# Kernel tuning notes

Hardware: AMD Instinct MI355X
Metric: run time of the kernel (lower is better)

The kernel has to match this reference:

```python
import jax, jax.numpy as jnp
import numpy as np

B, S, D = 128, 50, 128
NUM_NODE = 40000
HOP, N_ITER, SAMPLE = 2, 2, 12
N_NEI = 8
TEMP, MU, LEAK = 0.5, 0.1, 0.2


def setup_inputs() -> dict:
    key = jax.random.key(0)
    ks = jax.random.split(key, 32)
    stdv = 1.0 / np.sqrt(D)
    u = lambda k, shp: jax.random.uniform(k, shp, jnp.float32, -stdv, stdv)
    return {
        "inputs": jax.random.randint(ks[0], (B, S), 0, NUM_NODE),
        "adj": jax.random.randint(ks[1], (B, S, S), 0, 5),
        "item": jax.random.randint(ks[2], (B, S), 0, NUM_NODE),
        "simi_mask": jax.random.randint(ks[3], (B, S, S), 0, 2),
        "as_items_0": jax.random.randint(ks[4], (B, S, N_NEI), 0, NUM_NODE),
        "as_items_1": jax.random.randint(ks[5], (B, S, N_NEI), 0, NUM_NODE),
        "as_items_ssl_0": jax.random.randint(ks[6], (B, S, N_NEI), 0, NUM_NODE),
        "as_items_ssl_1": jax.random.randint(ks[7], (B, S, N_NEI), 0, NUM_NODE),
        "last_item_mask": jnp.zeros((B, S), bool).at[:, -1].set(True),
        "adj_all": jax.random.randint(ks[8], (NUM_NODE, SAMPLE), 0, NUM_NODE),
        "num": jax.random.uniform(ks[9], (NUM_NODE, SAMPLE)),
        "emb": u(ks[10], (NUM_NODE, D)),
        "pos_emb": u(ks[11], (200, D)),
        "a_local": u(ks[12], (N_ITER, 4, D)),
        "mir_w1": u(ks[13], (N_ITER, D, D)),
        "mir_w2": u(ks[14], (N_ITER, D, D)),
        "glob_w1": u(ks[15], (HOP, D + 1, D)),
        "glob_w2": u(ks[16], (HOP, D, 1)),
        "glob_w3": u(ks[17], (HOP, 2 * D, D)),
        "attr_w": u(ks[18], (2 * D, D)),
        "highway_w": u(ks[19], (2 * D, D)),
        "glu1_w": u(ks[20], (D, D)),
        "glu2_w": u(ks[21], (D, D)),
        "glu4_w": u(ks[22], (D, D)),
        "glu4_b": u(ks[23], (D,)),
        "w_s": u(ks[24], (D, 1)),
        "gate_w": u(ks[25], (2 * D, D)),
    }


def _forward(num, emb, pos_emb, a_local, mir_w1, mir_w2, glob_w1, glob_w2, glob_w3,
             attr_w, highway_w, glu1_w, glu2_w, glu4_w, glu4_b, w_s, gate_w,
             inputs, adj, item, simi_mask, as_lists, as_ssl_lists, last_item_mask, adj_all):
    mi = (inputs != 0).astype(emb.dtype)  # [B,S]
    h = emb[inputs]                        # [B,S,D]

    # ---- AttributeAggregator (masked-mean pool per attribute + gated fusion) ----
    def pool(idx_list):
        ps = []
        for idx in idx_list:
            m = (idx != 0).astype(emb.dtype)[..., None]  # [B,S,N,1]
            ps.append(jnp.sum(emb[idx] * m, 2) / (jnp.sum(m, 2) + 1e-8))
        return jnp.mean(jnp.stack(ps), 0)  # [B,S,D]
    hf1 = pool(as_lists)
    hf2 = pool(as_ssl_lists)
    g_attr = jax.nn.sigmoid(jnp.concatenate([h, hf1], -1) @ attr_w)
    hf = g_attr * h + (1.0 - g_attr) * hf1

    # ---- multi-hop neighbor sampling (irregular gathers) ----
    neigh = [inputs]
    wts = []
    for _ in range(HOP):
        flat = neigh[-1].reshape(-1)
        neigh.append(adj_all[flat].reshape(B, -1))
        wts.append(num[flat].reshape(B, -1))
    ev = [emb[n] for n in neigh]  # [B,S,D], [B,S*12,D], [B,S*144,D]

    item_emb = emb[item] * mi[..., None]
    sess = jnp.sum(item_emb, 1) / jnp.sum(mi, -1, keepdims=True)  # [B,D]

    # ---- GlobalAggregator stack (GCE-GNN style attention over sampled neighbors) ----
    for n_hop in range(HOP):
        nxt = []
        for hop in range(HOP - n_hop):
            sv = ev[hop]                                   # [B,M,D]
            nv = ev[hop + 1].reshape(B, -1, SAMPLE, D)     # [B,M,12,D]
            nw = wts[hop].reshape(B, -1, SAMPLE)           # [B,M,12]
            extra = jnp.broadcast_to(sess[:, None, None, :], nv.shape)
            a = jnp.concatenate([extra * nv, nw[..., None]], -1)  # [B,M,12,D+1]
            a = jax.nn.leaky_relu(a @ glob_w1[n_hop], LEAK)
            a = jax.nn.softmax((a @ glob_w2[n_hop])[..., 0], -1)[..., None]
            agg = jnp.sum(a * nv, -2)
            nxt.append(jnp.tanh(jnp.concatenate([sv, agg], -1) @ glob_w3[n_hop]))
        ev = nxt
    h_global = ev[0].reshape(B, S, D)

    # ---- LocalAggregator (edge-typed GAT) + MirrorAggregator (gated exchange) ----
    x = h
    mirror = hf
    for i in range(HOP):
        e = jax.nn.leaky_relu(jnp.einsum('bid,bjd,kd->kbij', x, x, a_local[i]), LEAK)
        att = jnp.full((B, S, S), -9e15, x.dtype)
        for k in range(4):
            att = jnp.where(adj == k + 1, e[k], att)
        x = jax.nn.softmax(att, -1) @ x
        gm = jax.nn.sigmoid(x @ mir_w1[i] + mirror @ mir_w2[i])
        x, mirror = gm * x + (1.0 - gm) * mirror, gm * mirror + (1.0 - gm) * x

    # ---- highway + last-item select ----
    g = jax.nn.sigmoid(jnp.concatenate([h, x], -1) @ highway_w)
    x_dot = g * h + (1.0 - g) * x
    h_local = jnp.sum(x_dot * last_item_mask[..., None].astype(x_dot.dtype), 1)  # [B,D]

    mask = mi[..., None]
    pos = pos_emb[:S][None]  # [1,S,D]
    bw = emb[1:]             # [NUM_NODE-1,D]
    hs = jnp.sum(h_global * mask, -2) / jnp.sum(mask, 1)  # [B,D]

    # ---- SSL pairwise similarity loss ----
    sim = jnp.einsum('bid,bjd->bij', hf1, hf2) / TEMP
    l = -jnp.log(jax.nn.softmax(sim, 2) + 1e-8)
    simi_loss = jnp.mean(jnp.sum(l * (simi_mask == 1), (1, 2)))

    # ---- attention-style GLU scoring ----
    hp = x_dot + pos
    nh = jax.nn.sigmoid(hp @ glu1_w + hs[:, None, :] @ glu2_w + h_local[:, None, :] @ glu4_w + glu4_b)
    beta = (nh @ w_s) * mask
    zg = jnp.sum(beta * hp, 1)  # [B,D]
    gf = jax.nn.sigmoid(jnp.concatenate([zg, h_local], -1) @ gate_w) * MU
    zh = gf * h_local + (1.0 - gf) * zg
    scores = zh @ bw.T  # [B, NUM_NODE-1]
    return simi_loss, scores


def reference(inputs, adj, item, simi_mask, as_items_0, as_items_1,
              as_items_ssl_0, as_items_ssl_1, last_item_mask, adj_all, num,
              emb, pos_emb, a_local, mir_w1, mir_w2, glob_w1, glob_w2, glob_w3,
              attr_w, highway_w, glu1_w, glu2_w, glu4_w, glu4_b, w_s, gate_w):
    return _forward(num, emb, pos_emb, a_local, mir_w1, mir_w2, glob_w1, glob_w2, glob_w3,
                    attr_w, highway_w, glu1_w, glu2_w, glu4_w, glu4_b, w_s, gate_w,
                    inputs, adj, item, simi_mask, [as_items_0, as_items_1],
                    [as_items_ssl_0, as_items_ssl_1], last_item_mask, adj_all)
```

## Files before the change

### kernel.cpp

```cpp
#include <hip/hip_runtime.h>
#include <hip/hip_bf16.h>
#include <type_traits>


#define B 128
#define S 50
#define D 128
#define SAMPLE 12
#define NNEI 8
#define NODES 40000
#define NSC (NODES - 1)
#define LEAK 0.2f
#define TEMPV 0.5f
#define MUV 0.1f
#define NEG_BIG -3.0e38f

typedef const float* fpp;
typedef float* fpw;
typedef unsigned short u16;
typedef __attribute__((ext_vector_type(8))) short bfrag8;
typedef __attribute__((ext_vector_type(4))) float f32x4;

__device__ __forceinline__ float sigm(float x) { return 1.f / (1.f + __expf(-x)); }
__device__ __forceinline__ float tanh_f(float x) { return 1.f - 2.f / (__expf(2.f * x) + 1.f); }
__device__ __forceinline__ float leaky(float x) { return x >= 0.f ? x : LEAK * x; }
__device__ __forceinline__ u16 f2bf(float v) {
  __hip_bfloat16 h = __float2bfloat16(v);
  return *reinterpret_cast<u16*>(&h);
}
__device__ __forceinline__ float lde(const float* p, long i) { return p[i]; }
__device__ __forceinline__ float lde(const u16* p, long i) {
  union { unsigned int u; float f; } c;
  c.u = ((unsigned int)p[i]) << 16;
  return c.f;
}

__global__ __launch_bounds__(256) void kprep_emb(fpp emb, u16* __restrict__ out) {
  long i = ((long)blockIdx.x * 256 + threadIdx.x) * 4;
  if (i + 3 >= (long)NODES * D) return;
  float4 v = *(const float4*)(emb + i);
  out[i + 0] = f2bf(v.x); out[i + 1] = f2bf(v.y);
  out[i + 2] = f2bf(v.z); out[i + 3] = f2bf(v.w);
}

__global__ __launch_bounds__(256) void kprep4(fpp gw1, fpp gw3,
                                              u16* __restrict__ p1a,
                                              u16* __restrict__ p1b,
                                              u16* __restrict__ p3a,
                                              u16* __restrict__ p3b) {
  int i = blockIdx.x * 256 + threadIdx.x;
  fpp W; u16* dst; int KS;
  if (i < 16384)      { W = gw1;             dst = p1a; KS = 4; }
  else if (i < 32768) { W = gw1 + 129 * 128; dst = p1b; KS = 4; i -= 16384; }
  else if (i < 65536) { W = gw3;             dst = p3a; KS = 8; i -= 32768; }
  else                { W = gw3 + 256 * 128; dst = p3b; KS = 8; i -= 65536; }
  int e = i & 7;
  int lane = (i >> 3) & 63;
  int rest = i >> 9;
  int ks = rest % KS, nt = rest / KS;
  int k = ks * 32 + ((lane >> 4) << 3) + e;
  int n = (nt << 4) + (lane & 15);
  dst[i] = f2bf(W[(long)k * 128 + n]);
}

template <typename ET>
__global__ __launch_bounds__(128) void k1_gather(
    const int* __restrict__ inputs, const int* __restrict__ as0,
// ... 20 lines not shown
  }
  float hf1v = 0.5f * (p[0] + p[1]);
  float hf2v = 0.5f * (p[2] + p[3]);
  h_s[d] = hv;
  hf1_s[d] = hf1v;
  __syncthreads();
  float acc = 0.f;
  for (int k = 0; k < D; k++)
    acc += h_s[k] * attr_w[(long)k * D + d] + hf1_s[k] * attr_w[(long)(D + k) * D + d];
  float g = sigm(acc);
  float hfv = g * hv + (1.f - g) * hf1v;
  long o = (long)bs * D + d;
  h[o] = hv; hf1[o] = hf1v; hf2[o] = hf2v; xA[o] = hv; mir[o] = hfv;
  if (d == 0) mi[bs] = (inp != 0) ? 1.f : 0.f;
}

__global__ __launch_bounds__(128) void k2_sess(const int* __restrict__ inputs,
                                               const int* __restrict__ item,
                                               fpp emb, fpw sess) {
  int b = blockIdx.x;
  int d = threadIdx.x;
  float acc = 0.f, ms = 0.f;
  for (int s = 0; s < S; s++) {
    int inp = inputs[b * S + s];
    float m = (inp != 0) ? 1.f : 0.f;
    int it = item[b * S + s];
    acc += emb[(long)it * D + d] * m;
    ms += m;
  }
  sess[(long)b * D + d] = acc / ms;
}

template <typename ET>
__global__ __launch_bounds__(128) void kG_global(
    const int* __restrict__ inputs, const int* __restrict__ adj_all,
    fpp num, const ET* __restrict__ emb, fpp sess,
    fpp W1a, fpp W2a, fpp W1b, fpp W2b, fpp W3b,
    const u16* __restrict__ p1a, const u16* __restrict__ p1b,
    const u16* __restrict__ p3a, const u16* __restrict__ p3b,
    fpw hg) {
  int bs = blockIdx.x;
  int b = bs / S;
  int d = threadIdx.x;
  int lane = d & 63;
  int w = d >> 6;
  int q = lane >> 4;
  int mrow = lane & 15;

  __shared__ __align__(16) u16 nvs_l[16 * 136];
  __shared__ __align__(16) u16 svagg_l[16 * 264];
  __shared__ __align__(16) float ev_l[13 * 128];
  __shared__ __align__(16) float agg1_l[128];
  __shared__ float red_l[2][16];
  __shared__ float nw_l[16];

#pragma unroll
  for (int r = 12; r < 16; r++) {
    nvs_l[r * 136 + d] = 0;
    if (d < 8) nvs_l[r * 136 + 128 + d] = 0;
  }
#pragma unroll
  for (int r = 13; r < 16; r++) {
    svagg_l[r * 264 + d] = 0;
    svagg_l[r * 264 + 128 + d] = 0;
    if (d < 8) svagg_l[r * 264 + 256 + d] = 0;
  }

  float sess_d = sess[(long)b * D + d];
  int src0 = __builtin_amdgcn_readfirstlane(inputs[bs]);
  int n1[SAMPLE];
#pragma unroll
  for (int j = 0; j < SAMPLE; j++)
    n1[j] = __builtin_amdgcn_readfirstlane(adj_all[(long)src0 * SAMPLE + j]);
  svagg_l[0 * 264 + d] = f2bf(lde(emb, (long)src0 * D + d));

  float w2A[4], wlA[4], w2B[4], wlB[4];
#pragma unroll
  for (int nt = 0; nt < 4; nt++) {
    int col = (w * 4 + nt) * 16 + mrow;
    w2A[nt] = W2a[col];
    wlA[nt] = W1a[(long)D * D + col];
    w2B[nt] = W2b[col];
    wlB[nt] = W1b[(long)D * D + col];
  }

  float pre[SAMPLE], pnw = 0.f;
  {
#pragma unroll
    for (int j = 0; j < SAMPLE; j++)
      pre[j] = lde(emb, (long)n1[j] * D + d);
    if (d < SAMPLE) pnw = num[(long)src0 * SAMPLE + d];
  }
  for (int u = 0; u < 13; u++) {
    if (d < SAMPLE) nw_l[d] = pnw;
    float nvreg[SAMPLE];
#pragma unroll
    for (int j = 0; j < SAMPLE; j++) {
      nvreg[j] = pre[j];
      nvs_l[j * 136 + d] = f2bf(pre[j] * sess_d);
    }
    if (u == 0) {
#pragma unroll
      for (int j = 0; j < SAMPLE; j++)
        svagg_l[(1 + j) * 264 + d] = f2bf(nvreg[j]);
    }
    __syncthreads();
    if (u < 12) {
      int srcn = n1[u];
#pragma unroll
      for (int j = 0; j < SAMPLE; j++) {
        int nj = __builtin_amdgcn_readfirstlane(adj_all[(long)srcn * SAMPLE + j]);
        pre[j] = lde(emb, (long)nj * D + d);
      }
      if (d < SAMPLE) pnw = num[(long)srcn * SAMPLE + d];
    }
    f32x4 acc[4];
#pragma unroll
    for (int nt = 0; nt < 4; nt++) acc[nt] = (f32x4){0.f, 0.f, 0.f, 0.f};
#pragma unroll
    for (int ks = 0; ks < 4; ks++) {
      bfrag8 a = *(const bfrag8*)(nvs_l + mrow * 136 + q * 8 + ks * 32);
      const u16* pb = p1a + (w * 16 + ks) * 512 + lane * 8;
#pragma unroll
      for (int nt = 0; nt < 4; nt++) {
        bfrag8 bb = *(const bfrag8*)(pb + nt * 2048);
        acc[nt] = __builtin_amdgcn_mfma_f32_16x16x32_bf16(a, bb, acc[nt], 0, 0, 0);
      }
    }
    float lp[4] = {0.f, 0.f, 0.f, 0.f};
    float nwq[4];
#pragma unroll
    for (int i = 0; i < 4; i++) nwq[i] = (q < 3) ? nw_l[q * 4 + i] : 0.f;
#pragma unroll
    for (int nt = 0; nt < 4; nt++)
#pragma unroll
      for (int i = 0; i < 4; i++)
        lp[i] += leaky(acc[nt][i] + nwq[i] * wlA[nt]) * w2A[nt];
#pragma unroll
    for (int off = 1; off <= 8; off <<= 1)
#pragma unroll
      for (int i = 0; i < 4; i++) lp[i] += __shfl_xor(lp[i], off, 64);
    if (mrow == 0 && q < 3) {
#pragma unroll
      for (int i = 0; i < 4; i++) red_l[w][q * 4 + i] = lp[i];
    }
    __syncthreads();
    float lg[SAMPLE];
#pragma unroll
    for (int j = 0; j < SAMPLE; j++) lg[j] = red_l[0][j] + red_l[1][j];
    float mx = lg[0];
#pragma unroll
    for (int j = 1; j < SAMPLE; j++) mx = fmaxf(mx, lg[j]);
    float se = 0.f;
#pragma unroll
    for (int j = 0; j < SAMPLE; j++) { lg[j] = __expf(lg[j] - mx); se += lg[j]; }
    float inv = 1.f / se;
    float aggd = 0.f;
#pragma unroll
    for (int j = 0; j < SAMPLE; j++) aggd += lg[j] * inv * nvreg[j];
    svagg_l[u * 264 + 128 + d] = f2bf(aggd);
  }
  __syncthreads();

  {
    f32x4 accB[4];
#pragma unroll
    for (int nt = 0; nt < 4; nt++) accB[nt] = (f32x4){0.f, 0.f, 0.f, 0.f};
#pragma unroll
    for (int ks = 0; ks < 8; ks++) {
      bfrag8 a = *(const bfrag8*)(svagg_l + mrow * 264 + q * 8 + ks * 32);
      const u16* pb = p3a + (w * 32 + ks) * 512 + lane * 8;
#pragma unroll
      for (int nt = 0; nt < 4; nt++) {
        bfrag8 bb = *(const bfrag8*)(pb + nt * 4096);
        accB[nt] = __builtin_amdgcn_mfma_f32_16x16x32_bf16(a, bb, accB[nt], 0, 0, 0);
      }
    }
#pragma unroll
    for (int nt = 0; nt < 4; nt++) {
      int col = (w * 4 + nt) * 16 + mrow;
#pragma unroll
      for (int i = 0; i < 4; i++) {
        int u2 = q * 4 + i;
        if (u2 < 13) ev_l[u2 * 128 + col] = tanh_f(accB[nt][i]);
      }
    }
    __syncthreads();
  }

  {
    float evreg[SAMPLE];
#pragma unroll
    for (int j = 0; j < SAMPLE; j++) {
      float e = ev_l[(1 + j) * 128 + d];
      evreg[j] = e;
      nvs_l[j * 136 + d] = f2bf(e * sess_d);
    }
    if (d < SAMPLE) nw_l[d] = num[(long)src0 * SAMPLE + d];
    __syncthreads();

    f32x4 acc[4];
#pragma unroll
    for (int nt = 0; nt < 4; nt++) acc[nt] = (f32x4){0.f, 0.f, 0.f, 0.f};
#pragma unroll
    for (int ks = 0; ks < 4; ks++) {
      bfrag8 a = *(const bfrag8*)(nvs_l + mrow * 136 + q * 8 + ks * 32);
      const u16* pb = p1b + (w * 16 + ks) * 512 + lane * 8;
#pragma unroll
      for (int nt = 0; nt < 4; nt++) {
        bfrag8 bb = *(const bfrag8*)(pb + nt * 2048);
        acc[nt] = __builtin_amdgcn_mfma_f32_16x16x32_bf16(a, bb, acc[nt], 0, 0, 0);
      }
    }
    float lp[4] = {0.f, 0.f, 0.f, 0.f};
    float nwq[4];
#pragma unroll
    for (int i = 0; i < 4; i++) nwq[i] = (q < 3) ? nw_l[q * 4 + i] : 0.f;
#pragma unroll
    for (int nt = 0; nt < 4; nt++)
#pragma unroll
      for (int i = 0; i < 4; i++)
        lp[i] += leaky(acc[nt][i] + nwq[i] * wlB[nt]) * w2B[nt];
#pragma unroll
    for (int off = 1; off <= 8; off <<= 1)
#pragma unroll
      for (int i = 0; i < 4; i++) lp[i] += __shfl_xor(lp[i], off, 64);
    if (mrow == 0 && q < 3) {
#pragma unroll
      for (int i = 0; i < 4; i++) red_l[w][q * 4 + i] = lp[i];
    }
    __syncthreads();

    float lg[SAMPLE];
#pragma unroll
    for (int j = 0; j < SAMPLE; j++) lg[j] = red_l[0][j] + red_l[1][j];
    float mx = lg[0];
#pragma unroll
    for (int j = 1; j < SAMPLE; j++) mx = fmaxf(mx, lg[j]);
    float se = 0.f;
#pragma unroll
    for (int j = 0; j < SAMPLE; j++) { lg[j] = __expf(lg[j] - mx); se += lg[j]; }
    float inv = 1.f / se;
    float agg1d = 0.f;
#pragma unroll
    for (int j = 0; j < SAMPLE; j++) agg1d += lg[j] * inv * evreg[j];
    agg1_l[d] = agg1d;
    __syncthreads();

    float accf = 0.f;
#pragma unroll 4
    for (int k4 = 0; k4 < 32; k4++) {
      float4 a4 = *(const float4*)&ev_l[4 * k4];
      float4 g4 = *(const float4*)&agg1_l[4 * k4];
      accf += a4.x * W3b[(4 * k4 + 0) * D + d] + a4.y * W3b[(4 * k4 + 1) * D + d] +
              a4.z * W3b[(4 * k4 + 2) * D + d] + a4.w * W3b[(4 * k4 + 3) * D + d] +
              g4.x * W3b[(D + 4 * k4 + 0) * D + d] + g4.y * W3b[(D + 4 * k4 + 1) * D + d] +
              g4.z * W3b[(D + 4 * k4 + 2) * D + d] + g4.w * W3b[(D + 4 * k4 + 3) * D + d];
    }
    hg[(long)bs * D + d] = tanh_f(accf);
  }
}

__global__ __launch_bounds__(128) void k5ab(fpp x, const int* __restrict__ adj,
                                            fpp a_loc, fpp w1, fpp w2,
                                            fpw xout, fpw mir,
                                            fpp hw, fpp h, fpw x_dot,
                                            float* __restrict__ h_local,
                                            int fin) {
  int b = blockIdx.x / S;
  int row = blockIdx.x % S;
  int tid = threadIdx.x;
  __shared__ float xi_s[D];
  __shared__ float ak_s[4][D];
  __shared__ float alpha_s[S];
  __shared__ float part_s[4][2][64];
  long idx = ((long)b * S + row) * D + tid;
  xi_s[tid] = x[idx];
#pragma unroll
  for (int k = 0; k < 4; k++) ak_s[k][tid] = a_loc[(long)k * D + tid];
  __syncthreads();
  {
    int j = tid & 63, hf = tid >> 6;
    float a0 = 0.f, a1 = 0.f, a2 = 0.f, a3 = 0.f;
    if (j < S) {
      const float* xj = x + ((long)b * S + j) * D + hf * 64;
      int off = hf * 64;
      for (int dd = 0; dd < 64; dd++) {
        float prod = xi_s[off + dd] * xj[dd];
        a0 += prod * ak_s[0][off + dd];
        a1 += prod * ak_s[1][off + dd];
        a2 += prod * ak_s[2][off + dd];
        a3 += prod * ak_s[3][off + dd];
      }
// ... 243 lines not shown
  fpp mir_w2 = (fpp)d_in[15];
  fpp gw1 = (fpp)d_in[16];
  fpp gw2 = (fpp)d_in[17];
  fpp gw3 = (fpp)d_in[18];
  fpp attr_w = (fpp)d_in[19];
  fpp highway_w = (fpp)d_in[20];
  fpp glu1 = (fpp)d_in[21];
  fpp glu2 = (fpp)d_in[22];
  fpp glu4 = (fpp)d_in[23];
  fpp glu4b = (fpp)d_in[24];
  fpp w_s = (fpp)d_in[25];
  fpp gate_w = (fpp)d_in[26];

  float* ob = (float*)d_out;
  constexpr long BSD_ = (long)B * S * D;
  fpw s_h = ob + 0 * BSD_;
  fpw s_hf1 = ob + 1 * BSD_;
  fpw s_hf2 = ob + 2 * BSD_;
  fpw s_mir = ob + 3 * BSD_;
  fpw s_xA = ob + 4 * BSD_;
  fpw s_xB = ob + 5 * BSD_;

  float* ws = (float*)d_ws;
  float* w_loss = ws + 0;
  float* w_mi = ws + 16;
  float* w_sess = w_mi + (long)B * S;
  float* w_hl = w_sess + (long)B * D;
  float* w_zh = w_hl + (long)B * D;
  u16* p1a = (u16*)(ws + 72000);
  u16* p1b = (u16*)(ws + 72000 + 8192);
  u16* p3a = (u16*)(ws + 72000 + 16384);
  u16* p3b = (u16*)(ws + 72000 + 32768);
  u16* embbf = (u16*)((char*)d_ws + 491520);
  bool useBF = ws_size >= (size_t)12 * 1024 * 1024;

  hipMemsetAsync((void*)w_loss, 0, sizeof(float), stream);

  kprep4<<<384, 256, 0, stream>>>(gw1, gw3, p1a, p1b, p3a, p3b);
  if (useBF)
    kprep_emb<<<(NODES * D / 4 + 255) / 256, 256, 0, stream>>>(emb, embbf);

  if (useBF)
    k1_gather<u16><<<B * S, 128, 0, stream>>>(inputs, as0, as1, ss0, ss1,
                                              embbf, attr_w, s_h, s_hf1, s_hf2,
                                              w_mi, s_xA, s_mir);
  else
    k1_gather<float><<<B * S, 128, 0, stream>>>(inputs, as0, as1, ss0, ss1,
                                                emb, attr_w, s_h, s_hf1, s_hf2,
                                                w_mi, s_xA, s_mir);
  k7_simi<<<B * S, 128, 0, stream>>>(s_hf1, s_hf2, simi_mask, w_loss);
  k2_sess<<<B, 128, 0, stream>>>(inputs, item, emb, w_sess);
  if (useBF)
    kG_global<u16><<<B * S, 128, 0, stream>>>(inputs, adj_all, num, embbf,
                                              w_sess, gw1, gw2,
                                              gw1 + 129 * 128, gw2 + 128,
                                              gw3 + 256 * 128, p1a, p1b, p3a,
                                              p3b, s_hf2 );
  else
    kG_global<float><<<B * S, 128, 0, stream>>>(inputs, adj_all, num, emb,
                                                w_sess, gw1, gw2,
                                                gw1 + 129 * 128, gw2 + 128,
                                                gw3 + 256 * 128, p1a, p1b, p3a,
                                                p3b, s_hf2 );
  k5ab<<<B * S, 128, 0, stream>>>(s_xA, adj, a_local, mir_w1, mir_w2,
                                  s_xB, s_mir, highway_w, s_h, s_hf1, w_hl, 0);
  k5ab<<<B * S, 128, 0, stream>>>(s_xB, adj, a_local + 4 * D,
                                  mir_w1 + (long)D * D, mir_w2 + (long)D * D,
                                  s_xA, s_mir, highway_w, s_h,
                                  s_hf1 , w_hl, 1);
  k8_glu<<<B, 512, 0, stream>>>(s_hf2 , s_hf1 , pos,
                                w_hl, w_mi, glu1, glu2, glu4, glu4b, w_s,
                                gate_w, w_zh);
  if (useBF)
    k9_scores<u16><<<(NSC + 63) / 64, 256, 0, stream>>>(w_zh, embbf, w_loss,
                                                        (float*)d_out);
  else
    k9_scores<float><<<(NSC + 63) / 64, 256, 0, stream>>>(w_zh, emb, w_loss,
                                                          (float*)d_out);
}
```

Baseline: 739.6 us.

## Restructure global aggregator kernel: 4 waves each own neighbor groups, prefetch indices

The global-graph kernel now runs 256 threads (4 waves). All second-hop neighbor indices and weights are prefetched into shared memory up front. Each wave independently processes a subset of the 13 neighbor groups with its own MFMA tile covering the full 128 output columns and a wave-local softmax, which removes the per-iteration block barriers. Gathered rows are loaded directly as bf16 MFMA fragments with double buffering, and the final linear layer is split across both thread halves. The cost is more registers per thread (launch bounds set to 3 blocks) and redundant weight-fragment loads per wave.

```diff
diff --git a/kernel.cpp b/kernel.cpp
--- a/kernel.cpp
+++ b/kernel.cpp
@@ -33,6 +33,37 @@
   union { unsigned int u; float f; } c;
   c.u = ((unsigned int)p[i]) << 16;
   return c.f;
+}
+__device__ __forceinline__ float bfu(short s) {
+  union { unsigned u; float f; } c;
+  c.u = ((unsigned)(unsigned short)s) << 16;
+  return c.f;
+}
+
+template <typename ET>
+__device__ __forceinline__ bfrag8 load_frag(const ET* __restrict__ emb, long row, int koff) {
+  if constexpr (sizeof(ET) == 2) {
+    return *(const bfrag8*)(const void*)(emb + row * D + koff);
+  } else {
+    const float* s = (const float*)(emb + row * D + koff);
+    float4 lo = *(const float4*)s;
+    float4 hi = *(const float4*)(s + 4);
+    bfrag8 b;
+    b[0] = (short)f2bf(lo.x); b[1] = (short)f2bf(lo.y);
+    b[2] = (short)f2bf(lo.z); b[3] = (short)f2bf(lo.w);
+    b[4] = (short)f2bf(hi.x); b[5] = (short)f2bf(hi.y);
+    b[6] = (short)f2bf(hi.z); b[7] = (short)f2bf(hi.w);
+    return b;
+  }
+}
+
+__device__ __forceinline__ bfrag8 scale8(bfrag8 r, float4 sa, float4 sb) {
+  bfrag8 o;
+  o[0] = (short)f2bf(bfu(r[0]) * sa.x); o[1] = (short)f2bf(bfu(r[1]) * sa.y);
+  o[2] = (short)f2bf(bfu(r[2]) * sa.z); o[3] = (short)f2bf(bfu(r[3]) * sa.w);
+  o[4] = (short)f2bf(bfu(r[4]) * sb.x); o[5] = (short)f2bf(bfu(r[5]) * sb.y);
+  o[6] = (short)f2bf(bfu(r[6]) * sb.z); o[7] = (short)f2bf(bfu(r[7]) * sb.w);
+  return o;
 }
 
 __global__ __launch_bounds__(256) void kprep_emb(fpp emb, u16* __restrict__ out) {
@@ -119,233 +150,246 @@
 }
 
 template <typename ET>
-__global__ __launch_bounds__(128) void kG_global(
+__global__ __launch_bounds__(256, 3) void kG_global(
     const int* __restrict__ inputs, const int* __restrict__ adj_all,
     fpp num, const ET* __restrict__ emb, fpp sess,
     fpp W1a, fpp W2a, fpp W1b, fpp W2b, fpp W3b,
     const u16* __restrict__ p1a, const u16* __restrict__ p1b,
-    const u16* __restrict__ p3a, const u16* __restrict__ p3b,
-    fpw hg) {
+    const u16* __restrict__ p3a, fpw hg) {
   int bs = blockIdx.x;
   int b = bs / S;
-  int d = threadIdx.x;
-  int lane = d & 63;
-  int w = d >> 6;
+  int t = threadIdx.x;
+  int lane = t & 63;
+  int w = t >> 6;
   int q = lane >> 4;
   int mrow = lane & 15;
 
-  __shared__ __align__(16) u16 nvs_l[16 * 136];
-  __shared__ __align__(16) u16 svagg_l[16 * 264];
-  __shared__ __align__(16) float ev_l[13 * 128];
+  __shared__ int n1_l[12];
+  __shared__ int idx_l[160];
+  __shared__ __align__(16) float nw_l[160];
+  __shared__ int svidx_l[16];
+  __shared__ __align__(16) u16 nvs_l[4][16 * 136];
+  __shared__ __align__(16) u16 agg_l[16 * 136];
+  __shared__ __align__(16) float ev_l[16 * 132];
+  __shared__ float red_l[64];
   __shared__ __align__(16) float agg1_l[128];
-  __shared__ float red_l[2][16];
-  __shared__ float nw_l[16];
-
-#pragma unroll
-  for (int r = 12; r < 16; r++) {
-    nvs_l[r * 136 + d] = 0;
-    if (d < 8) nvs_l[r * 136 + 128 + d] = 0;
-  }
-#pragma unroll
-  for (int r = 13; r < 16; r++) {
-    svagg_l[r * 264 + d] = 0;
-    svagg_l[r * 264 + 128 + d] = 0;
-    if (d < 8) svagg_l[r * 264 + 256 + d] = 0;
-  }
-
-  float sess_d = sess[(long)b * D + d];
-  int src0 = __builtin_amdgcn_readfirstlane(inputs[bs]);
-  int n1[SAMPLE];
-#pragma unroll
-  for (int j = 0; j < SAMPLE; j++)
-    n1[j] = __builtin_amdgcn_readfirstlane(adj_all[(long)src0 * SAMPLE + j]);
-  svagg_l[0 * 264 + d] = f2bf(lde(emb, (long)src0 * D + d));
-
-  float w2A[4], wlA[4], w2B[4], wlB[4];
-#pragma unroll
-  for (int nt = 0; nt < 4; nt++) {
-    int col = (w * 4 + nt) * 16 + mrow;
-    w2A[nt] = W2a[col];
-    wlA[nt] = W1a[(long)D * D + col];
-    w2B[nt] = W2b[col];
-    wlB[nt] = W1b[(long)D * D + col];
-  }
-
-  float pre[SAMPLE], pnw = 0.f;
+
+  int src0 = inputs[bs];
+  if (t < 12) n1_l[t] = adj_all[(long)src0 * SAMPLE + t];
+  if (t < 204) ((unsigned*)agg_l)[884 + t] = 0;
+  __syncthreads();
+  if (t < 156) {
+    int u = (t * 683) >> 13;
+    int j = t - u * 12;
+    int su = u ? n1_l[u - 1] : src0;
+    idx_l[t] = adj_all[(long)su * SAMPLE + j];
+    nw_l[t] = num[(long)su * SAMPLE + j];
+  } else if (t < 160) {
+    idx_l[t] = 0; nw_l[t] = 0.f;
+  } else if (t < 176) {
+    int m = t - 160;
+    svidx_l[m] = (m == 0) ? src0 : (m <= 12 ? n1_l[m - 1] : 0);
+  }
+  __syncthreads();
+
+  const float* sessb = sess + (long)b * D;
+  float wl8[8], w28[8];
+#pragma unroll
+  for (int nt = 0; nt < 8; nt++) {
+    int col = nt * 16 + mrow;
+    wl8[nt] = W1a[(long)D * D + col];
+    w28[nt] = W2a[col];
+  }
+  u16* nvsw = nvs_l[w];
+
+  bfrag8 rawA[4], rawB[4];
   {
-#pragma unroll
-    for (int j = 0; j < SAMPLE; j++)
-      pre[j] = lde(emb, (long)n1[j] * D + d);
-    if (d < SAMPLE) pnw = num[(long)src0 * SAMPLE + d];
-  }
-  for (int u = 0; u < 13; u++) {
-    if (d < SAMPLE) nw_l[d] = pnw;
-    float nvreg[SAMPLE];
-#pragma unroll
-    for (int j = 0; j < SAMPLE; j++) {
-      nvreg[j] = pre[j];
-      nvs_l[j * 136 + d] = f2bf(pre[j] * sess_d);
-    }
-    if (u == 0) {
-#pragma unroll
-      for (int j = 0; j < SAMPLE; j++)
-        svagg_l[(1 + j) * 264 + d] = f2bf(nvreg[j]);
-    }
-    __syncthreads();
-    if (u < 12) {
-      int srcn = n1[u];
-#pragma unroll
-      for (int j = 0; j < SAMPLE; j++) {
-        int nj = __builtin_amdgcn_readfirstlane(adj_all[(long)srcn * SAMPLE + j]);
-        pre[j] = lde(emb, (long)nj * D + d);
+    long ridx = idx_l[w * 12 + (mrow < 12 ? mrow : 0)];
+#pragma unroll
+    for (int ks = 0; ks < 4; ks++) rawA[ks] = load_frag(emb, ridx, ks * 32 + q * 8);
+  }
+  for (int u = w; u < 13; u += 4) {
+    int un = u + 4;
+    if (un < 13) {
+      long ridx = idx_l[un * 12 + (mrow < 12 ? mrow : 0)];
+#pragma unroll
+      for (int ks = 0; ks < 4; ks++) rawB[ks] = load_frag(emb, ridx, ks * 32 + q * 8);
+    }
+    f32x4 acc[8];
+#pragma unroll
+    for (int nt = 0; nt < 8; nt++) acc[nt] = (f32x4){0.f, 0.f, 0.f, 0.f};
+#pragma unroll
+    for (int ks = 0; ks < 4; ks++) {
+      float4 sa = *(const float4*)(sessb + ks * 32 + q * 8);
+      float4 sb = *(const float4*)(sessb + ks * 32 + q * 8 + 4);
+      bfrag8 a = scale8(rawA[ks], sa, sb);
+      const u16* pb = p1a + ks * 512 + lane * 8;
+#pragma unroll
+      for (int nt = 0; nt < 8; nt++)
+        acc[nt] = __builtin_amdgcn_mfma_f32_16x16x32_bf16(
+            a, *(const bfrag8*)(pb + nt * 2048), acc[nt], 0, 0, 0);
+    }
+    float4 nwq = *(const float4*)(nw_l + u * 12 + q * 4);
+    float lp[4] = {0.f, 0.f, 0.f, 0.f};
+#pragma unroll
+    for (int nt = 0; nt < 8; nt++) {
+      lp[0] += leaky(acc[nt][0] + nwq.x * wl8[nt]) * w28[nt];
+      lp[1] += leaky(acc[nt][1] + nwq.y * wl8[nt]) * w28[nt];
+      lp[2] += leaky(acc[nt][2] + nwq.z * wl8[nt]) * w28[nt];
+      lp[3] += leaky(acc[nt][3] + nwq.w * wl8[nt]) * w28[nt];
+    }
+#pragma unroll
+    for (int off = 1; off <= 8; off <<= 1)
+#pragma unroll
+      for (int i = 0; i < 4; i++) lp[i] += __shfl_xor(lp[i], off, 64);
+    float m4 = (q < 3) ? fmaxf(fmaxf(lp[0], lp[1]), fmaxf(lp[2], lp[3])) : NEG_BIG;
+    m4 = fmaxf(m4, __shfl_xor(m4, 16, 64));
+    m4 = fmaxf(m4, __shfl_xor(m4, 32, 64));
+    float e0 = 0.f, e1 = 0.f, e2 = 0.f, e3 = 0.f, ssum = 0.f;
+    if (q < 3) {
+      e0 = __expf(lp[0] - m4); e1 = __expf(lp[1] - m4);
+      e2 = __expf(lp[2] - m4); e3 = __expf(lp[3] - m4);
+      ssum = e0 + e1 + e2 + e3;
+    }
+    ssum += __shfl_xor(ssum, 16, 64);
+    ssum += __shfl_xor(ssum, 32, 64);
+    float inv = 1.f / ssum;
+    float al[4] = {e0 * inv, e1 * inv, e2 * inv, e3 * inv};
+    float aj[12];
+#pragma unroll
+    for (int j = 0; j < 12; j++) aj[j] = __shfl(al[j & 3], (j >> 2) << 4, 64);
+#pragma unroll
+    for (int ks = 0; ks < 4; ks++)
+      *(bfrag8*)(nvsw + mrow * 136 + ks * 32 + q * 8) = rawA[ks];
+    float a0 = 0.f, a1 = 0.f;
+#pragma unroll
+    for (int j = 0; j < 12; j++) {
+      unsigned pv = *(const unsigned*)(nvsw + j * 136 + lane * 2);
+      union { unsigned u; float f; } lo, hi;
+      lo.u = pv << 16; hi.u = pv & 0xffff0000u;
+      a0 += aj[j] * lo.f; a1 += aj[j] * hi.f;
+    }
+    unsigned pk = ((unsigned)f2bf(a1) << 16) | (unsigned)f2bf(a0);
+    *(unsigned*)(agg_l + u * 136 + lane * 2) = pk;
+#pragma unroll
+    for (int ks = 0; ks < 4; ks++) rawA[ks] = rawB[ks];
+  }
+  __syncthreads();
+
+  {
+    long svr = svidx_l[mrow];
+    f32x4 accB[2];
+    accB[0] = (f32x4){0.f, 0.f, 0.f, 0.f};
+    accB[1] = (f32x4){0.f, 0.f, 0.f, 0.f};
+#pragma unroll
+    for (int ks = 0; ks < 4; ks++) {
+      bfrag8 a = load_frag(emb, svr, ks * 32 + q * 8);
+      const u16* pb = p3a + ks * 512 + lane * 8;
+#pragma unroll
+      for (int n = 0; n < 2; n++)
+        accB[n] = __builtin_amdgcn_mfma_f32_16x16x32_bf16(
+            a, *(const bfrag8*)(pb + (w * 2 + n) * 4096), accB[n], 0, 0, 0);
+    }
+#pragma unroll
+    for (int ks = 4; ks < 8; ks++) {
+      bfrag8 a = *(const bfrag8*)(agg_l + mrow * 136 + (ks - 4) * 32 + q * 8);
+      const u16* pb = p3a + ks * 512 + lane * 8;
+#pragma unroll
+      for (int n = 0; n < 2; n++)
+        accB[n] = __builtin_amdgcn_mfma_f32_16x16x32_bf16(
+            a, *(const bfrag8*)(pb + (w * 2 + n) * 4096), accB[n], 0, 0, 0);
+    }
+#pragma unroll
+    for (int n = 0; n < 2; n++) {
+      int col = (w * 2 + n) * 16 + mrow;
+#pragma unroll
+      for (int i = 0; i < 4; i++) {
+        int row = q * 4 + i;
+        if (row < 13) ev_l[row * 132 + col] = tanh_f(accB[n][i]);
       }
-      if (d < SAMPLE) pnw = num[(long)srcn * SAMPLE + d];
-    }
-    f32x4 acc[4];
-#pragma unroll
-    for (int nt = 0; nt < 4; nt++) acc[nt] = (f32x4){0.f, 0.f, 0.f, 0.f};
+    }
+  }
+  __syncthreads();
+
+  {
+    float wlB[2], w2B[2];
+#pragma unroll
+    for (int n = 0; n < 2; n++) {
+      int col = (w * 2 + n) * 16 + mrow;
+      wlB[n] = W1b[(long)D * D + col];
+      w2B[n] = W2b[col];
+    }
+    int rr = 1 + (mrow < 12 ? mrow : 0);
+    f32x4 accC[2];
+    accC[0] = (f32x4){0.f, 0.f, 0.f, 0.f};
+    accC[1] = (f32x4){0.f, 0.f, 0.f, 0.f};
 #pragma unroll
     for (int ks = 0; ks < 4; ks++) {
-      bfrag8 a = *(const bfrag8*)(nvs_l + mrow * 136 + q * 8 + ks * 32);
-      const u16* pb = p1a + (w * 16 + ks) * 512 + lane * 8;
-#pragma unroll
-      for (int nt = 0; nt < 4; nt++) {
-        bfrag8 bb = *(const bfrag8*)(pb + nt * 2048);
-        acc[nt] = __builtin_amdgcn_mfma_f32_16x16x32_bf16(a, bb, acc[nt], 0, 0, 0);
-      }
-    }
-    float lp[4] = {0.f, 0.f, 0.f, 0.f};
-    float nwq[4];
-#pragma unroll
-    for (int i = 0; i < 4; i++) nwq[i] = (q < 3) ? nw_l[q * 4 + i] : 0.f;
-#pragma unroll
-    for (int nt = 0; nt < 4; nt++)
-#pragma unroll
-      for (int i = 0; i < 4; i++)
-        lp[i] += leaky(acc[nt][i] + nwq[i] * wlA[nt]) * w2A[nt];
+      float4 sa = *(const float4*)(sessb + ks * 32 + q * 8);
+      float4 sb = *(const float4*)(sessb + ks * 32 + q * 8 + 4);
+      float4 lo = *(const float4*)(ev_l + rr * 132 + ks * 32 + q * 8);
+      float4 hi = *(const float4*)(ev_l + rr * 132 + ks * 32 + q * 8 + 4);
+      bfrag8 a;
+      a[0] = (short)f2bf(lo.x * sa.x); a[1] = (short)f2bf(lo.y * sa.y);
+      a[2] = (short)f2bf(lo.z * sa.z); a[3] = (short)f2bf(lo.w * sa.w);
+      a[4] = (short)f2bf(hi.x * sb.x); a[5] = (short)f2bf(hi.y * sb.y);
+      a[6] = (short)f2bf(hi.z * sb.z); a[7] = (short)f2bf(hi.w * sb.w);
+      const u16* pb = p1b + ks * 512 + lane * 8;
+#pragma unroll
+      for (int n = 0; n < 2; n++)
+        accC[n] = __builtin_amdgcn_mfma_f32_16x16x32_bf16(
+            a, *(const bfrag8*)(pb + (w * 2 + n) * 2048), accC[n], 0, 0, 0);
+    }
+    float4 nwq0 = *(const float4*)(nw_l + q * 4);
+    float lp2[4] = {0.f, 0.f, 0.f, 0.f};
+#pragma unroll
+    for (int n = 0; n < 2; n++) {
+      lp2[0] += leaky(accC[n][0] + nwq0.x * wlB[n]) * w2B[n];
+      lp2[1] += leaky(accC[n][1] + nwq0.y * wlB[n]) * w2B[n];
+      lp2[2] += leaky(accC[n][2] + nwq0.z * wlB[n]) * w2B[n];
+      lp2[3] += leaky(accC[n][3] + nwq0.w * wlB[n]) * w2B[n];
+    }
 #pragma unroll
     for (int off = 1; off <= 8; off <<= 1)
 #pragma unroll
-      for (int i = 0; i < 4; i++) lp[i] += __shfl_xor(lp[i], off, 64);
-    if (mrow == 0 && q < 3) {
-#pragma unroll
-      for (int i = 0; i < 4; i++) red_l[w][q * 4 + i] = lp[i];
-    }
-    __syncthreads();
-    float lg[SAMPLE];
-#pragma unroll
-    for (int j = 0; j < SAMPLE; j++) lg[j] = red_l[0][j] + red_l[1][j];
+      for (int i = 0; i < 4; i++) lp2[i] += __shfl_xor(lp2[i], off, 64);
+    if (mrow == 0) {
+#pragma unroll
+      for (int i = 0; i < 4; i++) red_l[w * 16 + q * 4 + i] = lp2[i];
+    }
+  }
+  __syncthreads();
+  {
+    float lg[12];
+#pragma unroll
+    for (int j = 0; j < 12; j++)
+      lg[j] = red_l[j] + red_l[16 + j] + red_l[32 + j] + red_l[48 + j];
     float mx = lg[0];
 #pragma unroll
-    for (int j = 1; j < SAMPLE; j++) mx = fmaxf(mx, lg[j]);
+    for (int j = 1; j < 12; j++) mx = fmaxf(mx, lg[j]);
     float se = 0.f;
 #pragma unroll
-    for (int j = 0; j < SAMPLE; j++) { lg[j] = __expf(lg[j] - mx); se += lg[j]; }
-    float inv = 1.f / se;
-    float aggd = 0.f;
-#pragma unroll
-    for (int j = 0; j < SAMPLE; j++) aggd += lg[j] * inv * nvreg[j];
-    svagg_l[u * 264 + 128 + d] = f2bf(aggd);
-  }
-  __syncthreads();
-
+    for (int j = 0; j < 12; j++) { lg[j] = __expf(lg[j] - mx); se += lg[j]; }
+    float invc = 1.f / se;
+    if (t < 128) {
+      float ag = 0.f;
+#pragma unroll
+      for (int j = 0; j < 12; j++) ag += lg[j] * invc * ev_l[(1 + j) * 132 + t];
+      agg1_l[t] = ag;
+    }
+  }
+  __syncthreads();
   {
-    f32x4 accB[4];
-#pragma unroll
-    for (int nt = 0; nt < 4; nt++) accB[nt] = (f32x4){0.f, 0.f, 0.f, 0.f};
-#pragma unroll
-    for (int ks = 0; ks < 8; ks++) {
-      bfrag8 a = *(const bfrag8*)(svagg_l + mrow * 264 + q * 8 + ks * 32);
-      const u16* pb = p3a + (w * 32 + ks) * 512 + lane * 8;
-#pragma unroll
-      for (int nt = 0; nt < 4; nt++) {
-        bfrag8 bb = *(const bfrag8*)(pb + nt * 4096);
-        accB[nt] = __builtin_amdgcn_mfma_f32_16x16x32_bf16(a, bb, accB[nt], 0, 0, 0);
-      }
-    }
-#pragma unroll
-    for (int nt = 0; nt < 4; nt++) {
-      int col = (w * 4 + nt) * 16 + mrow;
-#pragma unroll
-      for (int i = 0; i < 4; i++) {
-        int u2 = q * 4 + i;
-        if (u2 < 13) ev_l[u2 * 128 + col] = tanh_f(accB[nt][i]);
-      }
-    }
-    __syncthreads();
-  }
-
-  {
-    float evreg[SAMPLE];
-#pragma unroll
-    for (int j = 0; j < SAMPLE; j++) {
-      float e = ev_l[(1 + j) * 128 + d];
-      evreg[j] = e;
-      nvs_l[j * 136 + d] = f2bf(e * sess_d);
-    }
-    if (d < SAMPLE) nw_l[d] = num[(long)src0 * SAMPLE + d];
-    __syncthreads();
-
-    f32x4 acc[4];
-#pragma unroll
-    for (int nt = 0; nt < 4; nt++) acc[nt] = (f32x4){0.f, 0.f, 0.f, 0.f};
-#pragma unroll
-    for (int ks = 0; ks < 4; ks++) {
-      bfrag8 a = *(const bfrag8*)(nvs_l + mrow * 136 + q * 8 + ks * 32);
-      const u16* pb = p1b + (w * 16 + ks) * 512 + lane * 8;
-#pragma unroll
-      for (int nt = 0; nt < 4; nt++) {
-        bfrag8 bb = *(const bfrag8*)(pb + nt * 2048);
-        acc[nt] = __builtin_amdgcn_mfma_f32_16x16x32_bf16(a, bb, acc[nt], 0, 0, 0);
-      }
-    }
-    float lp[4] = {0.f, 0.f, 0.f, 0.f};
-    float nwq[4];
-#pragma unroll
-    for (int i = 0; i < 4; i++) nwq[i] = (q < 3) ? nw_l[q * 4 + i] : 0.f;
-#pragma unroll
-    for (int nt = 0; nt < 4; nt++)
-#pragma unroll
-      for (int i = 0; i < 4; i++)
-        lp[i] += leaky(acc[nt][i] + nwq[i] * wlB[nt]) * w2B[nt];
-#pragma unroll
-    for (int off = 1; off <= 8; off <<= 1)
-#pragma unroll
-      for (int i = 0; i < 4; i++) lp[i] += __shfl_xor(lp[i], off, 64);
-    if (mrow == 0 && q < 3) {
-#pragma unroll
-      for (int i = 0; i < 4; i++) red_l[w][q * 4 + i] = lp[i];
-    }
-    __syncthreads();
-
-    float lg[SAMPLE];
-#pragma unroll
-    for (int j = 0; j < SAMPLE; j++) lg[j] = red_l[0][j] + red_l[1][j];
-    float mx = lg[0];
-#pragma unroll
-    for (int j = 1; j < SAMPLE; j++) mx = fmaxf(mx, lg[j]);
-    float se = 0.f;
-#pragma unroll
-    for (int j = 0; j < SAMPLE; j++) { lg[j] = __expf(lg[j] - mx); se += lg[j]; }
-    float inv = 1.f / se;
-    float agg1d = 0.f;
-#pragma unroll
-    for (int j = 0; j < SAMPLE; j++) agg1d += lg[j] * inv * evreg[j];
-    agg1_l[d] = agg1d;
-    __syncthreads();
-
+    int d = t & 127, hh = t >> 7;
+    const float* av = hh ? agg1_l : ev_l;
+    const float* Wp = W3b + (hh ? (long)128 * D : 0) + d;
     float accf = 0.f;
 #pragma unroll 4
-    for (int k4 = 0; k4 < 32; k4++) {
-      float4 a4 = *(const float4*)&ev_l[4 * k4];
-      float4 g4 = *(const float4*)&agg1_l[4 * k4];
-      accf += a4.x * W3b[(4 * k4 + 0) * D + d] + a4.y * W3b[(4 * k4 + 1) * D + d] +
-              a4.z * W3b[(4 * k4 + 2) * D + d] + a4.w * W3b[(4 * k4 + 3) * D + d] +
-              g4.x * W3b[(D + 4 * k4 + 0) * D + d] + g4.y * W3b[(D + 4 * k4 + 1) * D + d] +
-              g4.z * W3b[(D + 4 * k4 + 2) * D + d] + g4.w * W3b[(D + 4 * k4 + 3) * D + d];
-    }
-    hg[(long)bs * D + d] = tanh_f(accf);
-  }
+    for (int k = 0; k < 128; k++) accf += av[k] * Wp[(long)k * D];
+    ev_l[(14 + hh) * 132 + d] = accf;
+  }
+  __syncthreads();
+  if (t < 128) hg[(long)bs * D + t] = tanh_f(ev_l[14 * 132 + t] + ev_l[15 * 132 + t]);
 }
 
 __global__ __launch_bounds__(128) void k5ab(fpp x, const int* __restrict__ adj,
@@ -674,17 +718,17 @@
   k7_simi<<<B * S, 128, 0, stream>>>(s_hf1, s_hf2, simi_mask, w_loss);
   k2_sess<<<B, 128, 0, stream>>>(inputs, item, emb, w_sess);
   if (useBF)
-    kG_global<u16><<<B * S, 128, 0, stream>>>(inputs, adj_all, num, embbf,
+    kG_global<u16><<<B * S, 256, 0, stream>>>(inputs, adj_all, num, embbf,
                                               w_sess, gw1, gw2,
                                               gw1 + 129 * 128, gw2 + 128,
                                               gw3 + 256 * 128, p1a, p1b, p3a,
-                                              p3b, s_hf2 );
+                                              s_hf2 );
   else
-    kG_global<float><<<B * S, 128, 0, stream>>>(inputs, adj_all, num, emb,
+    kG_global<float><<<B * S, 256, 0, stream>>>(inputs, adj_all, num, emb,
                                                 w_sess, gw1, gw2,
                                                 gw1 + 129 * 128, gw2 + 128,
                                                 gw3 + 256 * 128, p1a, p1b, p3a,
-                                                p3b, s_hf2 );
+                                                s_hf2 );
   k5ab<<<B * S, 128, 0, stream>>>(s_xA, adj, a_local, mir_w1, mir_w2,
                                   s_xB, s_mir, highway_w, s_h, s_hf1, w_hl, 0);
   k5ab<<<B * S, 128, 0, stream>>>(s_xB, adj, a_local + 4 * D,
```

After: 1.160 ms. 56.9% more time.

## Split global aggregator into per-unit hop-1 kernel and post-processing kernel

Applied to the files above, without the earlier changes.

Replaces the monolithic global-aggregation kernel with two kernels. The first launches one 64-thread block per (session position, neighbor unit), 13 per position, to compute the first-hop neighbor attention and aggregation with MFMA, writing bf16 results to a workspace. The second consumes those results to do the second hop, softmax and output projection with 256-thread blocks. The aim is more parallelism and occupancy in exchange for an extra launch and a workspace round trip. The split path only runs when the workspace is at least 32 MB.

```diff
diff --git a/kernel.cpp b/kernel.cpp
--- a/kernel.cpp
+++ b/kernel.cpp
@@ -33,6 +33,37 @@
   union { unsigned int u; float f; } c;
   c.u = ((unsigned int)p[i]) << 16;
   return c.f;
+}
+__device__ __forceinline__ float bfu(short s) {
+  union { unsigned u; float f; } c;
+  c.u = ((unsigned)(unsigned short)s) << 16;
+  return c.f;
+}
+
+template <typename ET>
+__device__ __forceinline__ bfrag8 load_frag(const ET* __restrict__ emb, long row, int koff) {
+  if constexpr (sizeof(ET) == 2) {
+    return *(const bfrag8*)(const void*)(emb + row * D + koff);
+  } else {
+    const float* s = (const float*)(emb + row * D + koff);
+    float4 lo = *(const float4*)s;
+    float4 hi = *(const float4*)(s + 4);
+    bfrag8 b;
+    b[0] = (short)f2bf(lo.x); b[1] = (short)f2bf(lo.y);
+    b[2] = (short)f2bf(lo.z); b[3] = (short)f2bf(lo.w);
+    b[4] = (short)f2bf(hi.x); b[5] = (short)f2bf(hi.y);
+    b[6] = (short)f2bf(hi.z); b[7] = (short)f2bf(hi.w);
+    return b;
+  }
+}
+
+__device__ __forceinline__ bfrag8 scale8(bfrag8 r, float4 sa, float4 sb) {
+  bfrag8 o;
+  o[0] = (short)f2bf(bfu(r[0]) * sa.x); o[1] = (short)f2bf(bfu(r[1]) * sa.y);
+  o[2] = (short)f2bf(bfu(r[2]) * sa.z); o[3] = (short)f2bf(bfu(r[3]) * sa.w);
+  o[4] = (short)f2bf(bfu(r[4]) * sb.x); o[5] = (short)f2bf(bfu(r[5]) * sb.y);
+  o[6] = (short)f2bf(bfu(r[6]) * sb.z); o[7] = (short)f2bf(bfu(r[7]) * sb.w);
+  return o;
 }
 
 __global__ __launch_bounds__(256) void kprep_emb(fpp emb, u16* __restrict__ out) {
@@ -119,13 +150,256 @@
 }
 
 template <typename ET>
-__global__ __launch_bounds__(128) void kG_global(
+__global__ __launch_bounds__(64) void kGA_unit(
+    const int* __restrict__ inputs, const int* __restrict__ adj_all,
+    fpp num, const ET* __restrict__ emb, fpp sess,
+    fpp W1a, fpp W2a, const u16* __restrict__ p1a,
+    u16* __restrict__ aggws) {
+  int gb = blockIdx.x;
+  int bs = gb / 13;
+  int u = gb - bs * 13;
+  int b = bs / S;
+  int lane = threadIdx.x;
+  int q = lane >> 4;
+  int mrow = lane & 15;
+
+  __shared__ __align__(16) u16 nvs[16 * 136];
+
+  int src0 = inputs[bs];
+  int srcu = (u == 0) ? src0 : adj_all[(long)src0 * SAMPLE + (u - 1)];
+  int rid = adj_all[(long)srcu * SAMPLE + (mrow < 12 ? mrow : 0)];
+  float nwq[4];
+#pragma unroll
+  for (int i = 0; i < 4; i++)
+    nwq[i] = (q < 3) ? num[(long)srcu * SAMPLE + q * 4 + i] : 0.f;
+
+  const float* sessb = sess + (long)b * D;
+  bfrag8 rawA[4], sA[4];
+#pragma unroll
+  for (int ks = 0; ks < 4; ks++)
+    rawA[ks] = load_frag(emb, (long)rid, ks * 32 + q * 8);
+#pragma unroll
+  for (int ks = 0; ks < 4; ks++)
+    *(bfrag8*)(nvs + mrow * 136 + ks * 32 + q * 8) = rawA[ks];
+#pragma unroll
+  for (int ks = 0; ks < 4; ks++) {
+    float4 sa = *(const float4*)(sessb + ks * 32 + q * 8);
+    float4 sb = *(const float4*)(sessb + ks * 32 + q * 8 + 4);
+    sA[ks] = scale8(rawA[ks], sa, sb);
+  }
+  float wl8[8], w28[8];
+#pragma unroll
+  for (int nt = 0; nt < 8; nt++) {
+    int col = nt * 16 + mrow;
+    wl8[nt] = W1a[(long)D * D + col];
+    w28[nt] = W2a[col];
+  }
+  float lp[4] = {0.f, 0.f, 0.f, 0.f};
+#pragma unroll
+  for (int nt = 0; nt < 8; nt++) {
+    f32x4 acc = (f32x4){0.f, 0.f, 0.f, 0.f};
+#pragma unroll
+    for (int ks = 0; ks < 4; ks++)
+      acc = __builtin_amdgcn_mfma_f32_16x16x32_bf16(
+          sA[ks], *(const bfrag8*)(p1a + ks * 512 + lane * 8 + nt * 2048), acc, 0, 0, 0);
+    lp[0] += leaky(acc[0] + nwq[0] * wl8[nt]) * w28[nt];
+    lp[1] += leaky(acc[1] + nwq[1] * wl8[nt]) * w28[nt];
+    lp[2] += leaky(acc[2] + nwq[2] * wl8[nt]) * w28[nt];
+    lp[3] += leaky(acc[3] + nwq[3] * wl8[nt]) * w28[nt];
+  }
+#pragma unroll
+  for (int off = 1; off <= 8; off <<= 1)
+#pragma unroll
+    for (int i = 0; i < 4; i++) lp[i] += __shfl_xor(lp[i], off, 64);
+  float m4 = (q < 3) ? fmaxf(fmaxf(lp[0], lp[1]), fmaxf(lp[2], lp[3])) : NEG_BIG;
+  m4 = fmaxf(m4, __shfl_xor(m4, 16, 64));
+  m4 = fmaxf(m4, __shfl_xor(m4, 32, 64));
+  float e0 = 0.f, e1 = 0.f, e2 = 0.f, e3 = 0.f, ssum = 0.f;
+  if (q < 3) {
+    e0 = __expf(lp[0] - m4); e1 = __expf(lp[1] - m4);
+    e2 = __expf(lp[2] - m4); e3 = __expf(lp[3] - m4);
+    ssum = e0 + e1 + e2 + e3;
+  }
+  ssum += __shfl_xor(ssum, 16, 64);
+  ssum += __shfl_xor(ssum, 32, 64);
+  float inv = 1.f / ssum;
+  float al[4] = {e0 * inv, e1 * inv, e2 * inv, e3 * inv};
+  float aj[12];
+#pragma unroll
+  for (int j = 0; j < 12; j++) aj[j] = __shfl(al[j & 3], (j >> 2) << 4, 64);
+  float a0 = 0.f, a1 = 0.f;
+#pragma unroll
+  for (int j = 0; j < 12; j++) {
+    unsigned pv = *(const unsigned*)(nvs + j * 136 + lane * 2);
+    union { unsigned u; float f; } lo, hi;
+    lo.u = pv << 16; hi.u = pv & 0xffff0000u;
+    a0 += aj[j] * lo.f; a1 += aj[j] * hi.f;
+  }
+  unsigned pk = ((unsigned)f2bf(a1) << 16) | (unsigned)f2bf(a0);
+  *(unsigned*)(aggws + ((long)bs * 13 + u) * 128 + lane * 2) = pk;
+}
+
+template <typename ET>
+__global__ __launch_bounds__(256) void kGB_post(
+    const int* __restrict__ inputs, const int* __restrict__ adj_all,
+    fpp num, const ET* __restrict__ emb, fpp sess,
+    fpp W1b, fpp W2b, fpp W3b,
+    const u16* __restrict__ p1b, const u16* __restrict__ p3a,
+    const u16* __restrict__ aggws, fpw hg) {
+  int bs = blockIdx.x;
+  int b = bs / S;
+  int t = threadIdx.x;
+  int lane = t & 63;
+  int w = t >> 6;
+  int q = lane >> 4;
+  int mrow = lane & 15;
+
+  __shared__ int svidx_l[16];
+  __shared__ __align__(16) float ev_l[16 * 132];
+  __shared__ float red_l[64];
+  __shared__ __align__(16) float agg1_l[128];
+
+  int src0 = inputs[bs];
+  if (t < 16)
+    svidx_l[t] = (t == 0) ? src0 : (t <= 12 ? adj_all[(long)src0 * SAMPLE + t - 1] : 0);
+  __syncthreads();
+  const float* sessb = sess + (long)b * D;
+
+  {
+    long svr = svidx_l[mrow];
+    f32x4 accB[2];
+    accB[0] = (f32x4){0.f, 0.f, 0.f, 0.f};
+    accB[1] = (f32x4){0.f, 0.f, 0.f, 0.f};
+#pragma unroll
+    for (int ks = 0; ks < 4; ks++) {
+      bfrag8 a = load_frag(emb, svr, ks * 32 + q * 8);
+      const u16* pb = p3a + ks * 512 + lane * 8;
+#pragma unroll
+      for (int n = 0; n < 2; n++)
+        accB[n] = __builtin_amdgcn_mfma_f32_16x16x32_bf16(
+            a, *(const bfrag8*)(pb + (w * 2 + n) * 4096), accB[n], 0, 0, 0);
+    }
+#pragma unroll
+    for (int ks = 4; ks < 8; ks++) {
+      bfrag8 a;
+      if (mrow < 13)
+        a = *(const bfrag8*)(aggws + ((long)bs * 13 + mrow) * 128 + (ks - 4) * 32 + q * 8);
+      else
+        a = (bfrag8){0, 0, 0, 0, 0, 0, 0, 0};
+      const u16* pb = p3a + ks * 512 + lane * 8;
+#pragma unroll
+      for (int n = 0; n < 2; n++)
+        accB[n] = __builtin_amdgcn_mfma_f32_16x16x32_bf16(
+            a, *(const bfrag8*)(pb + (w * 2 + n) * 4096), accB[n], 0, 0, 0);
+    }
+#pragma unroll
+    for (int n = 0; n < 2; n++) {
+      int col = (w * 2 + n) * 16 + mrow;
+#pragma unroll
+      for (int i = 0; i < 4; i++) {
+        int row = q * 4 + i;
+        if (row < 13) ev_l[row * 132 + col] = tanh_f(accB[n][i]);
+      }
+    }
+  }
+  __syncthreads();
+
+  {
+    float wlB[2], w2B[2];
+#pragma unroll
+    for (int n = 0; n < 2; n++) {
+      int col = (w * 2 + n) * 16 + mrow;
+      wlB[n] = W1b[(long)D * D + col];
+      w2B[n] = W2b[col];
+    }
+    int rr = 1 + (mrow < 12 ? mrow : 0);
+    f32x4 accC[2];
+    accC[0] = (f32x4){0.f, 0.f, 0.f, 0.f};
+    accC[1] = (f32x4){0.f, 0.f, 0.f, 0.f};
+#pragma unroll
+    for (int ks = 0; ks < 4; ks++) {
+      float4 sa = *(const float4*)(sessb + ks * 32 + q * 8);
+      float4 sb = *(const float4*)(sessb + ks * 32 + q * 8 + 4);
+      float4 lo = *(const float4*)(ev_l + rr * 132 + ks * 32 + q * 8);
+      float4 hi = *(const float4*)(ev_l + rr * 132 + ks * 32 + q * 8 + 4);
+      bfrag8 a;
+      a[0] = (short)f2bf(lo.x * sa.x); a[1] = (short)f2bf(lo.y * sa.y);
+      a[2] = (short)f2bf(lo.z * sa.z); a[3] = (short)f2bf(lo.w * sa.w);
+      a[4] = (short)f2bf(hi.x * sb.x); a[5] = (short)f2bf(hi.y * sb.y);
+      a[6] = (short)f2bf(hi.z * sb.z); a[7] = (short)f2bf(hi.w * sb.w);
+      const u16* pb = p1b + ks * 512 + lane * 8;
+#pragma unroll
+      for (int n = 0; n < 2; n++)
+        accC[n] = __builtin_amdgcn_mfma_f32_16x16x32_bf16(
+            a, *(const bfrag8*)(pb + (w * 2 + n) * 2048), accC[n], 0, 0, 0);
+    }
+    float4 nwq0;
+    if (q < 3) {
+      nwq0.x = num[(long)src0 * SAMPLE + q * 4 + 0];
+      nwq0.y = num[(long)src0 * SAMPLE + q * 4 + 1];
+      nwq0.z = num[(long)src0 * SAMPLE + q * 4 + 2];
+      nwq0.w = num[(long)src0 * SAMPLE + q * 4 + 3];
+    } else {
+      nwq0.x = nwq0.y = nwq0.z = nwq0.w = 0.f;
+    }
+    float lp2[4] = {0.f, 0.f, 0.f, 0.f};
+#pragma unroll
+    for (int n = 0; n < 2; n++) {
+      lp2[0] += leaky(accC[n][0] + nwq0.x * wlB[n]) * w2B[n];
+      lp2[1] += leaky(accC[n][1] + nwq0.y * wlB[n]) * w2B[n];
+      lp2[2] += leaky(accC[n][2] + nwq0.z * wlB[n]) * w2B[n];
+      lp2[3] += leaky(accC[n][3] + nwq0.w * wlB[n]) * w2B[n];
+    }
+#pragma unroll
+    for (int off = 1; off <= 8; off <<= 1)
+#pragma unroll
+      for (int i = 0; i < 4; i++) lp2[i] += __shfl_xor(lp2[i], off, 64);
+    if (mrow == 0) {
+#pragma unroll
+      for (int i = 0; i < 4; i++) red_l[w * 16 + q * 4 + i] = lp2[i];
+    }
+  }
+  __syncthreads();
+  {
+    float lg[12];
+#pragma unroll
+    for (int j = 0; j < 12; j++)
+      lg[j] = red_l[j] + red_l[16 + j] + red_l[32 + j] + red_l[48 + j];
+    float mx = lg[0];
+#pragma unroll
+    for (int j = 1; j < 12; j++) mx = fmaxf(mx, lg[j]);
+    float se = 0.f;
+#pragma unroll
+    for (int j = 0; j < 12; j++) { lg[j] = __expf(lg[j] - mx); se += lg[j]; }
+    float invc = 1.f / se;
+    if (t < 128) {
+      float ag = 0.f;
+#pragma unroll
+      for (int j = 0; j < 12; j++) ag += lg[j] * invc * ev_l[(1 + j) * 132 + t];
+      agg1_l[t] = ag;
+    }
+  }
+  __syncthreads();
+  {
+    int d = t & 127, hh = t >> 7;
+    const float* av = hh ? agg1_l : ev_l;
+    const float* Wp = W3b + (hh ? (long)128 * D : 0) + d;
+    float accf = 0.f;
+#pragma unroll 4
+    for (int k = 0; k < 128; k++) accf += av[k] * Wp[(long)k * D];
+    ev_l[(14 + hh) * 132 + d] = accf;
+  }
+  __syncthreads();
+  if (t < 128) hg[(long)bs * D + t] = tanh_f(ev_l[14 * 132 + t] + ev_l[15 * 132 + t]);
+}
+
+template <typename ET>
+__global__ __launch_bounds__(128) void kG_mono(
     const int* __restrict__ inputs, const int* __restrict__ adj_all,
     fpp num, const ET* __restrict__ emb, fpp sess,
     fpp W1a, fpp W2a, fpp W1b, fpp W2b, fpp W3b,
     const u16* __restrict__ p1a, const u16* __restrict__ p1b,
-    const u16* __restrict__ p3a, const u16* __restrict__ p3b,
-    fpw hg) {
+    const u16* __restrict__ p3a, fpw hg) {
   int bs = blockIdx.x;
   int b = bs / S;
   int d = threadIdx.x;
@@ -655,7 +929,9 @@
   u16* p3a = (u16*)(ws + 72000 + 16384);
   u16* p3b = (u16*)(ws + 72000 + 32768);
   u16* embbf = (u16*)((char*)d_ws + 491520);
+  u16* aggws = (u16*)((char*)d_ws + 10731520);
   bool useBF = ws_size >= (size_t)12 * 1024 * 1024;
+  bool useSplit = useBF && ws_size >= ((size_t)32 << 20);
 
   hipMemsetAsync((void*)w_loss, 0, sizeof(float), stream);
 
@@ -673,18 +949,28 @@
                                                 w_mi, s_xA, s_mir);
   k7_simi<<<B * S, 128, 0, stream>>>(s_hf1, s_hf2, simi_mask, w_loss);
   k2_sess<<<B, 128, 0, stream>>>(inputs, item, emb, w_sess);
-  if (useBF)
-    kG_global<u16><<<B * S, 128, 0, stream>>>(inputs, adj_all, num, embbf,
+
+  if (useSplit) {
+    kGA_unit<u16><<<B * S * 13, 64, 0, stream>>>(inputs, adj_all, num, embbf,
+                                                 w_sess, gw1, gw2, p1a, aggws);
+    kGB_post<u16><<<B * S, 256, 0, stream>>>(inputs, adj_all, num, embbf,
+                                             w_sess, gw1 + 129 * 128, gw2 + 128,
+                                             gw3 + 256 * 128, p1b, p3a, aggws,
+                                             s_hf2 );
+  } else if (useBF) {
+    kG_mono<u16><<<B * S, 128, 0, stream>>>(inputs, adj_all, num, embbf,
+                                            w_sess, gw1, gw2,
+                                            gw1 + 129 * 128, gw2 + 128,
+                                            gw3 + 256 * 128, p1a, p1b, p3a,
+                                            s_hf2 );
+  } else {
+    kG_mono<float><<<B * S, 128, 0, stream>>>(inputs, adj_all, num, emb,
                                               w_sess, gw1, gw2,
                                               gw1 + 129 * 128, gw2 + 128,
                                               gw3 + 256 * 128, p1a, p1b, p3a,
-                                              p3b, s_hf2 );
-  else
-    kG_global<float><<<B * S, 128, 0, stream>>>(inputs, adj_all, num, emb,
-                                                w_sess, gw1, gw2,
-                                                gw1 + 129 * 128, gw2 + 128,
-                                                gw3 + 256 * 128, p1a, p1b, p3a,
-                                                p3b, s_hf2 );
+                                              s_hf2 );
+  }
+
   k5ab<<<B * S, 128, 0, stream>>>(s_xA, adj, a_local, mir_w1, mir_w2,
                                   s_xB, s_mir, highway_w, s_h, s_hf1, w_hl, 0);
   k5ab<<<B * S, 128, 0, stream>>>(s_xB, adj, a_local + 4 * D,
```

Measured after the change: 739.8 us. Within noise of the previous version (+0.0%).
